# Kernel tuning notes

Measured on AMD Instinct MI355X. Metric: run time of the kernel, lower is better.

Reference implementation:

```python
import jax, jax.numpy as jnp
import numpy as np

TEMPERATURE = 0.5


def setup_inputs() -> dict:
    key = jax.random.key(0)
    k1, k2 = jax.random.split(key)
    emb = jax.random.normal(k1, (16384, 128), dtype=jnp.float32)
    emb = emb / jnp.linalg.norm(emb, axis=1, keepdims=True)  # L2-normalized, per docstring
    labels = jax.random.randint(k2, (16384,), 0, 64, dtype=jnp.int64)
    return {"embeddings": emb, "partition_labels": labels}


def reference(embeddings, partition_labels):
    n = embeddings.shape[0]
    # [N, N] similarity matrix, scaled by temperature
    sim = jnp.matmul(embeddings, embeddings.T) / TEMPERATURE
    exp_sim = jnp.exp(sim)
    eye = jnp.eye(n, dtype=bool)
    pos_mask = (partition_labels[None, :] == partition_labels[:, None]) & ~eye
    # numerator: sum of exp over positives; denominator: sum over all k != i
    pos_sum = jnp.sum(jnp.where(pos_mask, exp_sim, 0.0), axis=1)
    all_sum = jnp.sum(jnp.where(~eye, exp_sim, 0.0), axis=1)
    valid = jnp.any(pos_mask, axis=1)
    loss_i = -(jnp.log(pos_sum) - jnp.log(all_sum))
    n_valid = jnp.sum(valid)
    total = jnp.sum(jnp.where(valid, loss_i, 0.0))
    return jnp.where(n_valid > 0, total / n_valid, 0.0)
```

## Files before the change

kernel.cpp:

```cpp
#include <hip/hip_runtime.h>

#define N_EMB 16384
#define DIM 128
#define BM 128
#define BN 128
#define NSPLIT 8
#define CPS (N_EMB / NSPLIT)
#define NCT (CPS / BN)

typedef __bf16 bf16x8 __attribute__((ext_vector_type(8)));
typedef float f32x4 __attribute__((ext_vector_type(4)));
typedef unsigned short us8 __attribute__((ext_vector_type(8)));
typedef unsigned int u32;

#define SCALE 2.8853900817779268f

__device__ inline float fast_exp2(float x) {
#if __has_builtin(__builtin_amdgcn_exp2f)
  return __builtin_amdgcn_exp2f(x);
#else
  return exp2f(x);
#endif
}
__device__ inline float fast_log2(float x) {
#if __has_builtin(__builtin_amdgcn_logf)
  return __builtin_amdgcn_logf(x);
#else
  return log2f(x);
#endif
}

__device__ inline unsigned short f2bf(float f) {
  unsigned int u = __float_as_uint(f);
  u += 0x7fffu + ((u >> 16) & 1u);
  return (unsigned short)(u >> 16);
}

__device__ inline void gll16(const unsigned short* g, unsigned short* l) {
  __builtin_amdgcn_global_load_lds(
      (const __attribute__((address_space(1))) u32*)g,
      (__attribute__((address_space(3))) u32*)l, 16, 0, 0);
}

__device__ inline void stage_tile_fl(const float* __restrict__ src,
                                     unsigned short* __restrict__ dst,
                                     int tid) {
#pragma unroll
  for (int i = 0; i < 8; ++i) {
    int G = i * 256 + tid;
    int col16 = G & 15;
    int quad = (G >> 4) & 3;
    int ks = (G >> 6) & 3;
    int tc = G >> 8;
    const float* p = src + (tc * 16 + col16) * DIM + ks * 32 + quad * 8;
    float4 a = *reinterpret_cast<const float4*>(p);
    float4 b = *reinterpret_cast<const float4*>(p + 4);
    us8 g;
    g[0] = f2bf(a.x); g[1] = f2bf(a.y); g[2] = f2bf(a.z); g[3] = f2bf(a.w);
    g[4] = f2bf(b.x); g[5] = f2bf(b.y); g[6] = f2bf(b.z); g[7] = f2bf(b.w);
    *reinterpret_cast<us8*>(dst + G * 8) = g;
  }
}

__global__ __launch_bounds__(256) void preconv(
    const float* __restrict__ emb, unsigned short* __restrict__ eraw,
    unsigned short* __restrict__ escal) {
  __shared__ unsigned short lds[128 * DIM];
  const int tid = threadIdx.x;
  const size_t base = (size_t)blockIdx.x * (128 * DIM);
  stage_tile_fl(emb + base, lds, tid);
  __syncthreads();
#pragma unroll
  for (int i = 0; i < 8; ++i) {
    int G = i * 256 + tid;
    us8 v = *reinterpret_cast<const us8*>(lds + G * 8);
    *reinterpret_cast<us8*>(eraw + base + G * 8) = v;
    us8 s;
#pragma unroll
    for (int j = 0; j < 8; ++j) {
      float f = __uint_as_float((u32)v[j] << 16) * SCALE;
      s[j] = f2bf(f);
    }
    *reinterpret_cast<us8*>(escal + base + G * 8) = s;
  }
}

__global__ __launch_bounds__(256, 4) void cl_main(
    const unsigned short* __restrict__ eraw,
    const unsigned short* __restrict__ escal,
    const int* __restrict__ labels, float* __restrict__ ws_all,
    float* __restrict__ ws_pos) {
  __shared__ unsigned short lds[BN * DIM];

  const int tid = threadIdx.x;
  const int lane = tid & 63;
  const int w = tid >> 6;
  const int col16 = lane & 15;
  const int quad = lane >> 4;
  const int r0 = blockIdx.x * BM;
  const int cs = blockIdx.y;

  {
    const unsigned short* g = escal + (size_t)r0 * DIM;
#pragma unroll
    for (int i = 0; i < 8; ++i) {
      int chunk = i * 4 + w;
      gll16(g + chunk * 512 + lane * 8, lds + chunk * 512);
    }
  }
  __syncthreads();

  bf16x8 afrag[2][4];
#pragma unroll
  for (int tr = 0; tr < 2; ++tr)
#pragma unroll
    for (int ks = 0; ks < 4; ++ks)
      afrag[tr][ks] = *reinterpret_cast<const bf16x8*>(
          lds + ((w * 2 + tr) * 4 + ks) * 512 + lane * 8);

  int labi[8];
  float all_p[8], pos_p[8];
#pragma unroll
  for (int t = 0; t < 8; ++t) {
    labi[t] = labels[r0 + w * 32 + (t >> 2) * 16 + quad * 4 + (t & 3)];
    all_p[t] = 0.f;
    pos_p[t] = 0.f;
  }

  for (int ct = 0; ct < NCT; ++ct) {
    const int c0 = cs * CPS + ct * BN;
    __syncthreads();
    {
      const unsigned short* g = eraw + (size_t)c0 * DIM;
#pragma unroll
      for (int i = 0; i < 8; ++i) {
        int chunk = i * 4 + w;
        gll16(g + chunk * 512 + lane * 8, lds + chunk * 512);
      }
    }
    __syncthreads();

#pragma unroll
    for (int tc = 0; tc < 8; ++tc) {
      bf16x8 bf[4];
#pragma unroll
      for (int ks = 0; ks < 4; ++ks)
        bf[ks] = *reinterpret_cast<const bf16x8*>(lds + (tc * 4 + ks) * 512 +
                                                  lane * 8);
      int labj = labels[c0 + tc * 16 + col16];
#pragma unroll
      for (int tr = 0; tr < 2; ++tr) {
        f32x4 acc = {0.f, 0.f, 0.f, 0.f};
#pragma unroll
        for (int ks = 0; ks < 4; ++ks)
          acc = __builtin_amdgcn_mfma_f32_16x16x32_bf16(afrag[tr][ks], bf[ks],
                                                        acc, 0, 0, 0);
        const bool diag = (c0 + tc * 16) == (r0 + w * 32 + tr * 16);
#pragma unroll
        for (int r = 0; r < 4; ++r) {
          float e = fast_exp2(acc[r]);
          if (diag && (quad * 4 + r) == col16) e = 0.f;
          all_p[tr * 4 + r] += e;
          pos_p[tr * 4 + r] += (labi[tr * 4 + r] == labj) ? e : 0.f;
        }
      }
    }
  }

#pragma unroll
  for (int t = 0; t < 8; ++t) {
    float a = all_p[t], p = pos_p[t];
#pragma unroll
    for (int m = 8; m >= 1; m >>= 1) {
      a += __shfl_xor(a, m, 64);
      p += __shfl_xor(p, m, 64);
    }
    if (col16 == 0) {
      int row_g = r0 + w * 32 + (t >> 2) * 16 + quad * 4 + (t & 3);
      ws_all[cs * N_EMB + row_g] = a;
      ws_pos[cs * N_EMB + row_g] = p;
    }
  }
}

__global__ __launch_bounds__(1024) void finalize_kernel(
    const float* __restrict__ ws_all, const float* __restrict__ ws_pos,
    float* __restrict__ out) {
  __shared__ float s_t[1024];
  __shared__ int s_c[1024];
  const int tid = threadIdx.x;
  float tot = 0.f;
  int cnt = 0;
  for (int row = tid; row < N_EMB; row += 1024) {
    float a = 0.f, p = 0.f;
#pragma unroll
    for (int s = 0; s < NSPLIT; ++s) {
      a += ws_all[s * N_EMB + row];
      p += ws_pos[s * N_EMB + row];
    }
    if (p > 0.f) {
      tot += fast_log2(a) - fast_log2(p);
      cnt++;
    }
  }
  s_t[tid] = tot;
  s_c[tid] = cnt;
  __syncthreads();
  for (int s = 512; s > 0; s >>= 1) {
    if (tid < s) {
      s_t[tid] += s_t[tid + s];
      s_c[tid] += s_c[tid + s];
    }
    __syncthreads();
  }
  if (tid == 0)
    out[0] =
        (s_c[0] > 0) ? (s_t[0] * 0.6931471805599453f / (float)s_c[0]) : 0.f;
}

extern "C" void kernel_launch(void* const* d_in, const int* in_sizes, int n_in,
                              void* d_out, int out_size, void* d_ws,
                              size_t ws_size, hipStream_t stream) {
  const float* emb = (const float*)d_in[0];
  const int* labels = (const int*)d_in[1];

  unsigned short* eraw = (unsigned short*)d_ws;
  unsigned short* escal = eraw + (size_t)N_EMB * DIM;
  float* ws_all = (float*)(escal + (size_t)N_EMB * DIM);
  float* ws_pos = ws_all + NSPLIT * N_EMB;

  preconv<<<N_EMB / 128, 256, 0, stream>>>(emb, eraw, escal);
  cl_main<<<dim3(N_EMB / BM, NSPLIT), 256, 0, stream>>>(eraw, escal, labels,
                                                        ws_all, ws_pos);
  finalize_kernel<<<1, 1024, 0, stream>>>(ws_all, ws_pos, (float*)d_out);
}
```

Measured before the change: 164.6 us.

## Sort rows by label into padded groups to replace per-element positive masking

Builds a label histogram and scatter permutation so embeddings are grouped by label with padding to 16-row groups. The main kernel then decides positives per 16-column block with a range test and drops the diagonal check. Diagonal, ghost and pad contributions are subtracted analytically in a row-reduction pass. This removes per-element label loads and compares in the hot loop, at the cost of about 6% more padded tiles, several extra kernel launches, and atomic-ordered permutation.

```diff
diff --git a/kernel.cpp b/kernel.cpp
--- a/kernel.cpp
+++ b/kernel.cpp
@@ -1,107 +1,124 @@
 #include <hip/hip_runtime.h>
 
-#define N_EMB 16384
+#define N_REAL 16384
+#define NLAB 64
+#define NP 17408
 #define DIM 128
-#define BM 128
-#define BN 128
 #define NSPLIT 8
-#define CPS (N_EMB / NSPLIT)
-#define NCT (CPS / BN)
+#define TILES_TOTAL (NP / 128)
+#define TPS (TILES_TOTAL / NSPLIT)
+#define GHOSTS (NP - N_REAL)
 
 typedef __bf16 bf16x8 __attribute__((ext_vector_type(8)));
 typedef float f32x4 __attribute__((ext_vector_type(4)));
 typedef unsigned short us8 __attribute__((ext_vector_type(8)));
+typedef unsigned short us;
 typedef unsigned int u32;
 
 #define SCALE 2.8853900817779268f
 
-__device__ inline float fast_exp2(float x) {
-#if __has_builtin(__builtin_amdgcn_exp2f)
-  return __builtin_amdgcn_exp2f(x);
-#else
-  return exp2f(x);
-#endif
-}
-__device__ inline float fast_log2(float x) {
-#if __has_builtin(__builtin_amdgcn_logf)
-  return __builtin_amdgcn_logf(x);
-#else
-  return log2f(x);
-#endif
-}
-
-__device__ inline unsigned short f2bf(float f) {
-  unsigned int u = __float_as_uint(f);
+__device__ inline float fast_exp2(float x) { return exp2f(x); }
+__device__ inline float fast_log2(float x) { return log2f(x); }
+
+__device__ inline us f2bf(float f) {
+  u32 u = __float_as_uint(f);
   u += 0x7fffu + ((u >> 16) & 1u);
-  return (unsigned short)(u >> 16);
-}
-
-__device__ inline void gll16(const unsigned short* g, unsigned short* l) {
+  return (us)(u >> 16);
+}
+__device__ inline float bf2f(us x) {
+  return __uint_as_float((u32)x << 16);
+}
+
+__device__ inline void gll16(const us* g, us* l) {
   __builtin_amdgcn_global_load_lds(
       (const __attribute__((address_space(1))) u32*)g,
       (__attribute__((address_space(3))) u32*)l, 16, 0, 0);
 }
 
-__device__ inline void stage_tile_fl(const float* __restrict__ src,
-                                     unsigned short* __restrict__ dst,
-                                     int tid) {
+
+__global__ void init_k(int* slab_p, float* total, int* count) {
+  int i = blockIdx.x * 256 + threadIdx.x;
+  if (i < NP) slab_p[i] = -1;
+  if (i == 0) { *total = 0.f; *count = 0; }
+}
+
+__global__ void hist_scan(const int* __restrict__ labels, int* cntg, int* offp,
+                          int* cursor) {
+  __shared__ int h[NLAB];
+  int tid = threadIdx.x;
+  if (tid < NLAB) h[tid] = 0;
+  __syncthreads();
+  for (int i = tid; i < N_REAL; i += 256) atomicAdd(&h[labels[i]], 1);
+  __syncthreads();
+  if (tid == 0) {
+    int o = 0;
+    for (int l = 0; l < NLAB; ++l) {
+      int c = h[l];
+      cntg[l] = c;
+      offp[l] = o;
+      cursor[l] = o;
+      o += (c + 15) & ~15;
+    }
+    offp[NLAB] = o;
+  }
+}
+
+__global__ void scatter_k(const int* __restrict__ labels, int* cursor,
+                          int* perm_p, int* slab_p) {
+  int i = blockIdx.x * 256 + threadIdx.x;
+  int l = labels[i];
+  int p = atomicAdd(&cursor[l], 1);
+  perm_p[p] = i;
+  slab_p[p] = l;
+}
+
+__global__ __launch_bounds__(256) void preconv(
+    const float* __restrict__ emb, const int* __restrict__ perm_p,
+    const int* __restrict__ slab_p, us* __restrict__ eraw,
+    us* __restrict__ escal) {
+  const int tid = threadIdx.x;
+  const size_t base = (size_t)blockIdx.x * 2048;
 #pragma unroll
   for (int i = 0; i < 8; ++i) {
-    int G = i * 256 + tid;
-    int col16 = G & 15;
-    int quad = (G >> 4) & 3;
-    int ks = (G >> 6) & 3;
-    int tc = G >> 8;
-    const float* p = src + (tc * 16 + col16) * DIM + ks * 32 + quad * 8;
-    float4 a = *reinterpret_cast<const float4*>(p);
-    float4 b = *reinterpret_cast<const float4*>(p + 4);
-    us8 g;
-    g[0] = f2bf(a.x); g[1] = f2bf(a.y); g[2] = f2bf(a.z); g[3] = f2bf(a.w);
-    g[4] = f2bf(b.x); g[5] = f2bf(b.y); g[6] = f2bf(b.z); g[7] = f2bf(b.w);
-    *reinterpret_cast<us8*>(dst + G * 8) = g;
-  }
-}
-
-__global__ __launch_bounds__(256) void preconv(
-    const float* __restrict__ emb, unsigned short* __restrict__ eraw,
-    unsigned short* __restrict__ escal) {
-  __shared__ unsigned short lds[128 * DIM];
-  const int tid = threadIdx.x;
-  const size_t base = (size_t)blockIdx.x * (128 * DIM);
-  stage_tile_fl(emb + base, lds, tid);
-  __syncthreads();
-#pragma unroll
-  for (int i = 0; i < 8; ++i) {
-    int G = i * 256 + tid;
-    us8 v = *reinterpret_cast<const us8*>(lds + G * 8);
-    *reinterpret_cast<us8*>(eraw + base + G * 8) = v;
-    us8 s;
-#pragma unroll
-    for (int j = 0; j < 8; ++j) {
-      float f = __uint_as_float((u32)v[j] << 16) * SCALE;
-      s[j] = f2bf(f);
-    }
-    *reinterpret_cast<us8*>(escal + base + G * 8) = s;
+    int g = i * 256 + tid;
+    int col16 = g & 15;
+    int quad = (g >> 4) & 3;
+    int ks = (g >> 6) & 3;
+    int tc = g >> 8;
+    int slot = blockIdx.x * 128 + tc * 16 + col16;
+    us8 r = {0, 0, 0, 0, 0, 0, 0, 0};
+    us8 sc = {0, 0, 0, 0, 0, 0, 0, 0};
+    if (slab_p[slot] >= 0) {
+      const float* p = emb + (size_t)perm_p[slot] * DIM + ks * 32 + quad * 8;
+      float4 a = *reinterpret_cast<const float4*>(p);
+      float4 b = *reinterpret_cast<const float4*>(p + 4);
+      r[0] = f2bf(a.x); r[1] = f2bf(a.y); r[2] = f2bf(a.z); r[3] = f2bf(a.w);
+      r[4] = f2bf(b.x); r[5] = f2bf(b.y); r[6] = f2bf(b.z); r[7] = f2bf(b.w);
+      sc[0] = f2bf(a.x * SCALE); sc[1] = f2bf(a.y * SCALE);
+      sc[2] = f2bf(a.z * SCALE); sc[3] = f2bf(a.w * SCALE);
+      sc[4] = f2bf(b.x * SCALE); sc[5] = f2bf(b.y * SCALE);
+      sc[6] = f2bf(b.z * SCALE); sc[7] = f2bf(b.w * SCALE);
+    }
+    *reinterpret_cast<us8*>(eraw + (base + g) * 8) = r;
+    *reinterpret_cast<us8*>(escal + (base + g) * 8) = sc;
   }
 }
 
 __global__ __launch_bounds__(256, 4) void cl_main(
-    const unsigned short* __restrict__ eraw,
-    const unsigned short* __restrict__ escal,
-    const int* __restrict__ labels, float* __restrict__ ws_all,
-    float* __restrict__ ws_pos) {
-  __shared__ unsigned short lds[BN * DIM];
+    const us* __restrict__ eraw, const us* __restrict__ escal,
+    const int* __restrict__ slab_p, const int* __restrict__ offp,
+    float* __restrict__ ws_all, float* __restrict__ ws_pos) {
+  __shared__ us lds[128 * DIM];
 
   const int tid = threadIdx.x;
   const int lane = tid & 63;
   const int w = tid >> 6;
-  const int col16 = lane & 15;
   const int quad = lane >> 4;
-  const int r0 = blockIdx.x * BM;
+  const int r0 = blockIdx.x * 128;
   const int cs = blockIdx.y;
 
   {
-    const unsigned short* g = escal + (size_t)r0 * DIM;
+    const us* g = escal + (size_t)blockIdx.x * (128 * DIM);
 #pragma unroll
     for (int i = 0; i < 8; ++i) {
       int chunk = i * 4 + w;
@@ -118,20 +135,23 @@
       afrag[tr][ks] = *reinterpret_cast<const bf16x8*>(
           lds + ((w * 2 + tr) * 4 + ks) * 512 + lane * 8);
 
-  int labi[8];
+  int lo[2], hi[2];
+#pragma unroll
+  for (int tr = 0; tr < 2; ++tr) {
+    int l = slab_p[r0 + w * 32 + tr * 16];
+    lo[tr] = (l >= 0) ? offp[l] : 0;
+    hi[tr] = (l >= 0) ? offp[l + 1] : 0;
+  }
+
   float all_p[8], pos_p[8];
 #pragma unroll
-  for (int t = 0; t < 8; ++t) {
-    labi[t] = labels[r0 + w * 32 + (t >> 2) * 16 + quad * 4 + (t & 3)];
-    all_p[t] = 0.f;
-    pos_p[t] = 0.f;
-  }
-
-  for (int ct = 0; ct < NCT; ++ct) {
-    const int c0 = cs * CPS + ct * BN;
+  for (int t = 0; t < 8; ++t) { all_p[t] = 0.f; pos_p[t] = 0.f; }
+
+  for (int ct = 0; ct < TPS; ++ct) {
+    const int ctg = cs * TPS + ct;
     __syncthreads();
     {
-      const unsigned short* g = eraw + (size_t)c0 * DIM;
+      const us* g = eraw + (size_t)ctg * (128 * DIM);
 #pragma unroll
       for (int i = 0; i < 8; ++i) {
         int chunk = i * 4 + w;
@@ -147,7 +167,7 @@
       for (int ks = 0; ks < 4; ++ks)
         bf[ks] = *reinterpret_cast<const bf16x8*>(lds + (tc * 4 + ks) * 512 +
                                                   lane * 8);
-      int labj = labels[c0 + tc * 16 + col16];
+      const int c = ctg * 128 + tc * 16;
 #pragma unroll
       for (int tr = 0; tr < 2; ++tr) {
         f32x4 acc = {0.f, 0.f, 0.f, 0.f};
@@ -155,13 +175,12 @@
         for (int ks = 0; ks < 4; ++ks)
           acc = __builtin_amdgcn_mfma_f32_16x16x32_bf16(afrag[tr][ks], bf[ks],
                                                         acc, 0, 0, 0);
-        const bool diag = (c0 + tc * 16) == (r0 + w * 32 + tr * 16);
+        const float m = (c >= lo[tr] && c < hi[tr]) ? 1.f : 0.f;
 #pragma unroll
         for (int r = 0; r < 4; ++r) {
           float e = fast_exp2(acc[r]);
-          if (diag && (quad * 4 + r) == col16) e = 0.f;
           all_p[tr * 4 + r] += e;
-          pos_p[tr * 4 + r] += (labi[tr * 4 + r] == labj) ? e : 0.f;
+          pos_p[tr * 4 + r] = fmaf(e, m, pos_p[tr * 4 + r]);
         }
       }
     }
@@ -175,47 +194,77 @@
       a += __shfl_xor(a, m, 64);
       p += __shfl_xor(p, m, 64);
     }
-    if (col16 == 0) {
+    if ((lane & 15) == 0) {
       int row_g = r0 + w * 32 + (t >> 2) * 16 + quad * 4 + (t & 3);
-      ws_all[cs * N_EMB + row_g] = a;
-      ws_pos[cs * N_EMB + row_g] = p;
-    }
-  }
-}
-
-__global__ __launch_bounds__(1024) void finalize_kernel(
+      ws_all[cs * NP + row_g] = a;
+      ws_pos[cs * NP + row_g] = p;
+    }
+  }
+}
+
+__global__ __launch_bounds__(256) void reduce_rows(
     const float* __restrict__ ws_all, const float* __restrict__ ws_pos,
-    float* __restrict__ out) {
-  __shared__ float s_t[1024];
-  __shared__ int s_c[1024];
+    const int* __restrict__ slab_p, const int* __restrict__ offp,
+    const int* __restrict__ cntg, const us* __restrict__ eraw,
+    const us* __restrict__ escal, float* total, int* count) {
+  __shared__ float s_t[256];
+  __shared__ int s_c[256];
   const int tid = threadIdx.x;
-  float tot = 0.f;
-  int cnt = 0;
-  for (int row = tid; row < N_EMB; row += 1024) {
+  const int s = blockIdx.x * 256 + tid;
+  float t = 0.f;
+  int c = 0;
+  int l = slab_p[s];
+  if (l >= 0) {
     float a = 0.f, p = 0.f;
 #pragma unroll
-    for (int s = 0; s < NSPLIT; ++s) {
-      a += ws_all[s * N_EMB + row];
-      p += ws_pos[s * N_EMB + row];
-    }
-    if (p > 0.f) {
-      tot += fast_log2(a) - fast_log2(p);
-      cnt++;
-    }
-  }
-  s_t[tid] = tot;
-  s_c[tid] = cnt;
-  __syncthreads();
-  for (int s = 512; s > 0; s >>= 1) {
-    if (tid < s) {
-      s_t[tid] += s_t[tid + s];
-      s_c[tid] += s_c[tid + s];
+    for (int k = 0; k < NSPLIT; ++k) {
+      a += ws_all[k * NP + s];
+      p += ws_pos[k * NP + s];
+    }
+    const int tile = s >> 7, rl = s & 127, tc = rl >> 4, c16 = rl & 15;
+    const us* pa = escal + (size_t)tile * (128 * DIM);
+    const us* pb = eraw + (size_t)tile * (128 * DIM);
+    float dot = 0.f;
+#pragma unroll
+    for (int ks = 0; ks < 4; ++ks)
+#pragma unroll
+      for (int q = 0; q < 4; ++q) {
+        int g = tc * 256 + ks * 64 + q * 16 + c16;
+        us8 va = *reinterpret_cast<const us8*>(pa + g * 8);
+        us8 vb = *reinterpret_cast<const us8*>(pb + g * 8);
+#pragma unroll
+        for (int j = 0; j < 8; ++j) dot = fmaf(bf2f(va[j]), bf2f(vb[j]), dot);
+      }
+    float eii = fast_exp2(dot);
+    a -= (float)GHOSTS + eii;
+    int pads = (offp[l + 1] - offp[l]) - cntg[l];
+    p -= (float)pads + eii;
+    if (cntg[l] > 1) {
+      t = fast_log2(a) - fast_log2(p);
+      c = 1;
+    }
+  }
+  s_t[tid] = t;
+  s_c[tid] = c;
+  __syncthreads();
+  for (int st = 128; st > 0; st >>= 1) {
+    if (tid < st) {
+      s_t[tid] += s_t[tid + st];
+      s_c[tid] += s_c[tid + st];
     }
     __syncthreads();
   }
-  if (tid == 0)
+  if (tid == 0) {
+    atomicAdd(total, s_t[0]);
+    atomicAdd(count, s_c[0]);
+  }
+}
+
+__global__ void final_k(const float* total, const int* count,
+                        float* __restrict__ out) {
+  if (threadIdx.x == 0)
     out[0] =
-        (s_c[0] > 0) ? (s_t[0] * 0.6931471805599453f / (float)s_c[0]) : 0.f;
+        (*count > 0) ? (*total) * 0.6931471805599453f / (float)(*count) : 0.f;
 }
 
 extern "C" void kernel_launch(void* const* d_in, const int* in_sizes, int n_in,
@@ -224,13 +273,26 @@
   const float* emb = (const float*)d_in[0];
   const int* labels = (const int*)d_in[1];
 
-  unsigned short* eraw = (unsigned short*)d_ws;
-  unsigned short* escal = eraw + (size_t)N_EMB * DIM;
-  float* ws_all = (float*)(escal + (size_t)N_EMB * DIM);
-  float* ws_pos = ws_all + NSPLIT * N_EMB;
-
-  preconv<<<N_EMB / 128, 256, 0, stream>>>(emb, eraw, escal);
-  cl_main<<<dim3(N_EMB / BM, NSPLIT), 256, 0, stream>>>(eraw, escal, labels,
-                                                        ws_all, ws_pos);
-  finalize_kernel<<<1, 1024, 0, stream>>>(ws_all, ws_pos, (float*)d_out);
-}
+  char* w = (char*)d_ws;
+  us* eraw = (us*)w;                      w += (size_t)NP * DIM * 2;
+  us* escal = (us*)w;                     w += (size_t)NP * DIM * 2;
+  float* ws_all = (float*)w;              w += (size_t)NSPLIT * NP * 4;
+  float* ws_pos = (float*)w;              w += (size_t)NSPLIT * NP * 4;
+  int* perm_p = (int*)w;                  w += NP * 4;
+  int* slab_p = (int*)w;                  w += NP * 4;
+  int* offp = (int*)w;                    w += (NLAB + 1) * 4;
+  int* cntg = (int*)w;                    w += NLAB * 4;
+  int* cursor = (int*)w;                  w += NLAB * 4;
+  float* total = (float*)w;               w += 16;
+  int* count = (int*)w;
+
+  init_k<<<(NP + 255) / 256, 256, 0, stream>>>(slab_p, total, count);
+  hist_scan<<<1, 256, 0, stream>>>(labels, cntg, offp, cursor);
+  scatter_k<<<N_REAL / 256, 256, 0, stream>>>(labels, cursor, perm_p, slab_p);
+  preconv<<<TILES_TOTAL, 256, 0, stream>>>(emb, perm_p, slab_p, eraw, escal);
+  cl_main<<<dim3(TILES_TOTAL, NSPLIT), 256, 0, stream>>>(eraw, escal, slab_p,
+                                                         offp, ws_all, ws_pos);
+  reduce_rows<<<NP / 256, 256, 0, stream>>>(ws_all, ws_pos, slab_p, offp, cntg,
+                                            eraw, escal, total, count);
+  final_k<<<1, 64, 0, stream>>>(total, count, (float*)d_out);
+}
```

Result: slower. 351.2 us (+113.4%).
